# Performance work log

Measured on AMD Instinct MI355X. Metric: run time of the kernel, lower is better.

The kernel has to match this reference:

```python
import jax, jax.numpy as jnp
import numpy as np

H = 8                 # num_heads
SCALE = 25.0          # self.scale
SIM_THRESH = 0.75
CONF_SIM_THRESH = 0.99


def _l2n(x):
    return x / jnp.linalg.norm(x, axis=-1, keepdims=True)


def setup_inputs() -> dict:
    key = jax.random.key(0)
    ks = jax.random.split(key, 10)
    B, N1, N2, C = 1, 512, 2048, 1024
    s = 0.02
    return {
        'x_cls': jax.random.normal(ks[0], (B, N2, C), jnp.float32),
        'x_reg': jax.random.normal(ks[1], (B, N2, C), jnp.float32),
        'cls_score': jax.random.uniform(ks[2], (N2,), dtype=jnp.float32),
        'fg_score': jax.random.uniform(ks[3], (N2,), dtype=jnp.float32),
        'W_q_cls': jax.random.normal(ks[4], (C, C), jnp.float32) * s,
        'W_kv_cls': jax.random.normal(ks[5], (C, 2 * C), jnp.float32) * s,
        'W_q_reg': jax.random.normal(ks[6], (C, C), jnp.float32) * s,
        'W_kv_reg': jax.random.normal(ks[7], (C, 2 * C), jnp.float32) * s,
        'W_lin': jax.random.normal(ks[8], (2 * C, 2 * C), jnp.float32) * s,
        'b_lin': jnp.zeros((2 * C,), jnp.float32),
        'W_lin_reg': jax.random.normal(ks[9], (2 * C, 2 * C), jnp.float32) * s,
        'b_lin_reg': jnp.zeros((2 * C,), jnp.float32),
        'local_preds_num': 512,
    }


def _forward(x_cls, x_reg, cls_score, fg_score, W_q_cls, W_kv_cls, W_q_reg, W_kv_reg,
             W_lin, b_lin, W_lin_reg, b_lin_reg, N1):
    B, N2, C = x_cls.shape
    hd = C // H
    # QKV projections (torch Linear with bias=False; weights stored [in,out])
    q_cls = (x_cls[:, :N1] @ W_q_cls).reshape(B, N1, H, hd).transpose(0, 2, 1, 3)   # [B,H,N1,hd]
    kv = (x_cls @ W_kv_cls).reshape(B, N2, 2, H, hd).transpose(2, 0, 3, 1, 4)
    k_cls, v_cls = kv[0], kv[1]                                                      # [B,H,N2,hd]
    q_reg = (x_reg[:, :N1] @ W_q_reg).reshape(B, N1, H, hd).transpose(0, 2, 1, 3)
    kv = (x_reg @ W_kv_reg).reshape(B, N2, 2, H, hd).transpose(2, 0, 3, 1, 4)
    k_reg, v_reg = kv[0], kv[1]
    # L2 normalization of q, k and of v for raw similarity
    q_cls, k_cls = _l2n(q_cls), _l2n(k_cls)
    q_reg, k_reg = _l2n(q_reg), _l2n(k_reg)
    v_cls_n, v_reg_n = _l2n(v_cls), _l2n(v_reg)
    # per-key score broadcast over [1,H,N1,N2] (use_mask=False path)
    cs = cls_score.reshape(1, 1, 1, N2)
    # raw value-value similarity
    attn_cls_raw = jnp.einsum('bhqd,bhkd->bhqk', v_cls_n[:, :, :N1], v_cls_n)        # [B,H,N1,N2]
    attn_reg_raw = jnp.einsum('bhqd,bhkd->bhqk', v_reg_n[:, :, :N1], v_reg_n)
    # blended softmax attention (attn_drop=0 -> identity)
    attn_cls = jax.nn.softmax(jnp.einsum('bhqd,bhkd->bhqk', q_cls, k_cls) * SCALE * cs, axis=-1)
    attn_reg = jax.nn.softmax(jnp.einsum('bhqd,bhkd->bhqk', q_reg, k_reg) * SCALE, axis=-1)
    attn = (attn_cls + attn_reg) * 0.5
    # attended features + original local values, then output linears
    x = jnp.einsum('bhqk,bhkd->bhqd', attn, v_cls).transpose(0, 2, 1, 3).reshape(B, N1, C)
    x_ori = v_cls[:, :, :N1].transpose(0, 2, 1, 3).reshape(B, N1, C)
    out_cls = jnp.concatenate([x, x_ori], axis=-1) @ W_lin + b_lin                   # [B,N1,2C]
    xr = jnp.einsum('bhqk,bhkd->bhqd', attn, v_reg).transpose(0, 2, 1, 3).reshape(B, N1, C)
    xr_ori = v_reg[:, :, :N1].transpose(0, 2, 1, 3).reshape(B, N1, C)
    out_reg = jnp.concatenate([xr, xr_ori], axis=-1) @ W_lin_reg + b_lin_reg         # reconf=True
    # ave branch: similarity-masked renormalized second-round averaging (batch 0)
    sim_mask = (attn_cls_raw.sum(axis=1)[0] / H > SIM_THRESH).astype(x_cls.dtype)    # [N1,N2]
    obj_mask = (attn_reg_raw.sum(axis=1)[0] / H > CONF_SIM_THRESH).astype(x_cls.dtype)
    sim_round2 = jax.nn.softmax(attn.sum(axis=1)[0] / H, axis=-1)
    sim_round2 = sim_mask * sim_round2
    sim_round2 = sim_round2 / sim_round2.sum(axis=-1, keepdims=True)
    obj_w = obj_mask * sim_round2
    obj_w = obj_w / obj_w.sum(axis=-1, keepdims=True)
    support_cls = v_cls.transpose(0, 2, 1, 3).reshape(B, N2, C)[0]                   # [N2,C]
    support_reg = v_reg.transpose(0, 2, 1, 3).reshape(B, N2, C)[0]
    cls_feature = jnp.concatenate([sim_round2 @ support_cls, out_cls[0]], axis=-1)   # [N1,3C]
    reg_feature = jnp.concatenate([obj_w @ support_reg, out_reg[0]], axis=-1)        # [N1,3C]
    return cls_feature, reg_feature


def reference(x_cls, x_reg, cls_score, fg_score, W_q_cls, W_kv_cls, W_q_reg, W_kv_reg,
              W_lin, b_lin, W_lin_reg, b_lin_reg, local_preds_num):
    return _forward(x_cls, x_reg, cls_score, fg_score, W_q_cls, W_kv_cls, W_q_reg,
                    W_kv_reg, W_lin, b_lin, W_lin_reg, b_lin_reg, local_preds_num)
```

## Files before the change

kernel.cpp:

```cpp
#include <hip/hip_runtime.h>

typedef _Float16 half8 __attribute__((ext_vector_type(8)));
typedef _Float16 half4v __attribute__((ext_vector_type(4)));
typedef float f32x4 __attribute__((ext_vector_type(4)));

#define GLD16(gptr, lptr) \
    __builtin_amdgcn_global_load_lds((const __attribute__((address_space(1))) void*)(gptr), \
                                     (__attribute__((address_space(3))) void*)(lptr), 16, 0, 0)

#define WAIT_VM3   0x0F73
#define WAIT_VM0   0x0F70
#define WAIT_LGKM0 0xC07F

struct GD {
    const _Float16* A; const _Float16* B; void* C;
    const float* colScale;
    _Float16 *vnp, *vtp, *xop;
    long sAh, sAg, sBh, sBg, sSplit, sCh, sCg;
    int lda, ldb, ldc, K, SK, hmask, hshift;
    int ahx, outHalf, csMode, nx, ny, normMode;
    float alpha;
};

__global__ __launch_bounds__(512, 4)
void hgemm3(GD d0, GD d1, int zSplit)
{
    const bool second = (int)blockIdx.z >= zSplit;
    const GD& d = second ? d1 : d0;
    const int bz = second ? (int)blockIdx.z - zSplit : (int)blockIdx.z;
    if ((int)blockIdx.x >= d.nx || (int)blockIdx.y >= d.ny) return;

    __shared__ uint4 smem[4608];
    char* sb = (char*)smem;
    const int tid = threadIdx.x;
    const int w = tid >> 6, l = tid & 63;
    const int m0 = blockIdx.y << 8, n0 = blockIdx.x << 7;
    const int wm = (w >> 1) << 6, wn = (w & 1) << 6;
    const int kq = l >> 4, lm = l & 15;

    const int zz = bz / d.SK, s = bz - zz * d.SK;
    const int h = d.ahx ? (int)blockIdx.x : (zz & d.hmask);
    const int g = d.ahx ? zz : (zz >> d.hshift);
    const _Float16* A = d.A + (long)h * d.sAh + (long)g * d.sAg;
    const _Float16* B = d.B + (long)h * d.sBh + (long)g * d.sBg;
    const long Coff = (long)s * d.sSplit + (long)h * d.sCh + (long)g * d.sCg;
    const int kper = d.K / d.SK, kbeg = s * kper;
    const int NT = kper >> 5;

    const int rS = (w << 4) + (l >> 2);
    const int cS = (l & 3) ^ ((l >> 3) & 3);
    const _Float16* gA0 = A + (long)(m0 + rS) * d.lda + kbeg + cS * 8;
    const _Float16* gB0 = B + (long)(n0 + rS) * d.ldb + kbeg + cS * 8;
    const int lo = w * 1024 + l * 16;

    auto stage = [&](int t) {
        char* dst = sb + (t % 3) * 24576;
        GLD16(gA0 + t * 32,                     dst + lo);
        GLD16(gA0 + (long)128 * d.lda + t * 32, dst + 8192 + lo);
        GLD16(gB0 + t * 32,                     dst + 16384 + lo);
    };

    f32x4 acc[4][4] = {};
    stage(0);
    if (NT > 1) stage(1);
    if (NT > 1) __builtin_amdgcn_s_waitcnt(WAIT_VM3);
    else        __builtin_amdgcn_s_waitcnt(WAIT_VM0);
    __builtin_amdgcn_s_barrier();

    const int sw16 = ((kq ^ ((lm >> 1) & 3)) << 4);
    for (int t = 0; t < NT; ++t) {
        const char* cb = sb + (t % 3) * 24576;
        half8 af[4], bfr[4];
        const char* pa = cb + (wm + lm) * 64 + sw16;
        const char* pb = cb + 16384 + (wn + lm) * 64 + sw16;
        #pragma unroll
        for (int i = 0; i < 4; ++i) {
            af[i]  = *(const half8*)(pa + i * 1024);
            bfr[i] = *(const half8*)(pb + i * 1024);
        }
        #pragma unroll
        for (int mi = 0; mi < 4; ++mi)
            #pragma unroll
            for (int ni = 0; ni < 4; ++ni)
                acc[mi][ni] = __builtin_amdgcn_mfma_f32_16x16x32_f16(af[mi], bfr[ni], acc[mi][ni], 0, 0, 0);
        __builtin_amdgcn_s_waitcnt(WAIT_LGKM0);
        if (t + 2 < NT) { stage(t + 2); __builtin_amdgcn_s_waitcnt(WAIT_VM3); }
        else if (t + 1 < NT) __builtin_amdgcn_s_waitcnt(WAIT_VM0);
        __builtin_amdgcn_s_barrier();
    }

    if (d.normMode == 0) {
        const int rbase = m0 + wm + kq * 4;
        #pragma unroll
        for (int mi = 0; mi < 4; ++mi) {
            #pragma unroll
            for (int ni = 0; ni < 4; ++ni) {
                const int col = n0 + wn + ni * 16 + lm;
                float cs = d.alpha;
                if (d.csMode == 1 || (d.csMode == 2 && g == 0)) cs *= d.colScale[col];
                #pragma unroll
                for (int r = 0; r < 4; ++r) {
                    const long row = rbase + mi * 16 + r;
                    const float v = acc[mi][ni][r] * cs;
                    const long off = Coff + row * d.ldc + col;
                    if (d.outHalf) ((_Float16*)d.C)[off] = (_Float16)v;
                    else           ((float*)d.C)[off] = v;
                }
            }
        }
        return;
    }

    float* part = (float*)sb;
    float ssq[4][4];
    #pragma unroll
    for (int mi = 0; mi < 4; ++mi)
        #pragma unroll
        for (int r = 0; r < 4; ++r) {
            float sq = 0.f;
            #pragma unroll
            for (int ni = 0; ni < 4; ++ni) { const float v = acc[mi][ni][r]; sq += v * v; }
            sq += __shfl_xor(sq, 1, 64);
            sq += __shfl_xor(sq, 2, 64);
            sq += __shfl_xor(sq, 4, 64);
            sq += __shfl_xor(sq, 8, 64);
            ssq[mi][r] = sq;
        }
    if (lm == 0) {
        #pragma unroll
        for (int mi = 0; mi < 4; ++mi)
            #pragma unroll
            for (int r = 0; r < 4; ++r)
                part[(w & 1) * 256 + wm + kq * 4 + mi * 16 + r] = ssq[mi][r];
    }
    __syncthreads();

    #pragma unroll
    for (int mi = 0; mi < 4; ++mi) {
        #pragma unroll
        for (int r = 0; r < 4; ++r) {
            const int rl = wm + kq * 4 + mi * 16 + r;
            const float inv = rsqrtf(part[rl] + part[256 + rl]);
            const long rg = m0 + rl;
            if (d.normMode == 1) {
                #pragma unroll
                for (int ni = 0; ni < 4; ++ni) {
                    const int col = n0 + wn + ni * 16 + lm;
                    ((_Float16*)d.C)[(long)g * 524288 + rg * 1024 + col] =
                        (_Float16)(acc[mi][ni][r] * inv);
                }
            } else if (n0 < 1024) {
                #pragma unroll
                for (int ni = 0; ni < 4; ++ni) {
                    const int col = n0 + wn + ni * 16 + lm;
                    ((_Float16*)d.C)[(long)g * 2097152 + rg * 1024 + col] =
                        (_Float16)(acc[mi][ni][r] * inv);
                }
            } else {
                #pragma unroll
                for (int ni = 0; ni < 4; ++ni) {
                    const int nL = n0 - 1024 + wn + ni * 16 + lm;
                    d.vnp[(long)g * 2097152 + rg * 1024 + nL] =
                        (_Float16)(acc[mi][ni][r] * inv);
                    if (rg < 512)
                        d.xop[(long)g * 524288 + rg * 1024 + nL] = (_Float16)acc[mi][ni][r];
                }
            }
        }
    }
    if (d.normMode == 2 && n0 >= 1024) {
        #pragma unroll
        for (int mi = 0; mi < 4; ++mi)
            #pragma unroll
            for (int ni = 0; ni < 4; ++ni) {
                const int nL = n0 - 1024 + wn + ni * 16 + lm;
                half4v t;
                t.x = (_Float16)acc[mi][ni][0]; t.y = (_Float16)acc[mi][ni][1];
                t.z = (_Float16)acc[mi][ni][2]; t.w = (_Float16)acc[mi][ni][3];
                *(half4v*)(d.vtp + (long)g * 2097152 + (long)nL * 2048
                           + m0 + wm + kq * 4 + mi * 16) = t;
            }
    }
}

static GD mkgd(const _Float16* A, const _Float16* B, void* C, const float* cscale,
               long sAh, long sAg, long sBh, long sBg, long sSplit, long sCh, long sCg,
               int lda, int ldb, int ldc, int K, int SK, int hmask, int hshift,
               int ahx, int outHalf, int csMode, int nx, int ny, float alpha)
{
    GD d; d.A=A; d.B=B; d.C=C; d.colScale=cscale;
    d.vnp=nullptr; d.vtp=nullptr; d.xop=nullptr;
    d.sAh=sAh; d.sAg=sAg; d.sBh=sBh; d.sBg=sBg; d.sSplit=sSplit; d.sCh=sCh; d.sCg=sCg;
    d.lda=lda; d.ldb=ldb; d.ldc=ldc; d.K=K; d.SK=SK; d.hmask=hmask; d.hshift=hshift;
    d.ahx=ahx; d.outHalf=outHalf; d.csMode=csMode; d.nx=nx; d.ny=ny; d.normMode=0;
    d.alpha=alpha;
    return d;
}

__global__ __launch_bounds__(256)
void cast_f2h(const float* __restrict__ s0, const float* __restrict__ s1,
              _Float16* __restrict__ d, int n4)
{
    const int i = blockIdx.x * 256 + threadIdx.x;
    const float* s = blockIdx.y ? s1 : s0;
    const float4 v = ((const float4*)s)[i];
    half4v o;
    o.x = (_Float16)v.x; o.y = (_Float16)v.y; o.z = (_Float16)v.z; o.w = (_Float16)v.w;
    ((half4v*)(d + (size_t)blockIdx.y * n4 * 4))[i] = o;
}

__global__ __launch_bounds__(256)
void prep_transpose(const float* __restrict__ Wq_c, const float* __restrict__ Wq_r,
                    const float* __restrict__ Wkv_c, const float* __restrict__ Wkv_r,
                    const float* __restrict__ Wl_c, const float* __restrict__ Wl_r,
                    _Float16* __restrict__ WqT, _Float16* __restrict__ WkvT,
                    _Float16* __restrict__ WlinT)
{
    __shared__ float t[32][33];
    const int z = blockIdx.z;
    const float* src; _Float16* dst; int ldsrc, lddst, nx, ky;
    switch (z) {
        case 0: src=Wq_c;  dst=WqT;            ldsrc=1024; lddst=1024; nx=32; ky=32; break;
        case 1: src=Wq_r;  dst=WqT+1048576;    ldsrc=1024; lddst=1024; nx=32; ky=32; break;
        case 2: src=Wkv_c; dst=WkvT;           ldsrc=2048; lddst=1024; nx=64; ky=32; break;
        case 3: src=Wkv_r; dst=WkvT+2097152;   ldsrc=2048; lddst=1024; nx=64; ky=32; break;
        case 4: src=Wl_c;  dst=WlinT;          ldsrc=2048; lddst=2048; nx=64; ky=64; break;
        default:src=Wl_r;  dst=WlinT+4194304;  ldsrc=2048; lddst=2048; nx=64; ky=64; break;
    }
    if ((int)blockIdx.x >= nx || (int)blockIdx.y >= ky) return;
    const int n0 = blockIdx.x << 5, k0 = blockIdx.y << 5;
    const int tx = threadIdx.x & 31, ty = threadIdx.x >> 5;
    #pragma unroll
    for (int j = ty; j < 32; j += 8)
        t[j][tx] = src[(size_t)(k0 + j) * ldsrc + n0 + tx];
    __syncthreads();
    #pragma unroll
    for (int j = ty; j < 32; j += 8)
        dst[(size_t)(n0 + j) * lddst + k0 + tx] = (_Float16)t[tx][j];
}

template<int OP>
__device__ __forceinline__ float bred(float v, float* lds)
{
    #pragma unroll
    for (int o = 32; o > 0; o >>= 1) {
        const float u = __shfl_xor(v, o, 64);
        v = OP ? fmaxf(v, u) : v + u;
    }
    __syncthreads();
    if ((threadIdx.x & 63) == 0) lds[threadIdx.x >> 6] = v;
    __syncthreads();
    return OP ? fmaxf(fmaxf(lds[0], lds[1]), fmaxf(lds[2], lds[3]))
              : lds[0] + lds[1] + lds[2] + lds[3];
}

__global__ __launch_bounds__(256)
void sb2_kernel(const _Float16* __restrict__ S16, const float* __restrict__ simPart,
                _Float16* __restrict__ attn,
                _Float16* __restrict__ wc, _Float16* __restrict__ wr)
{
    __shared__ float lds[4];
    const int q = blockIdx.x, t = threadIdx.x;
    float asum[8] = {};
    for (int hh = 0; hh < 8; ++hh) {
        const size_t rb = (size_t)(hh * 512 + q) * 2048;
        float vc[8], vr[8];
        float mc = -1e30f, mr = -1e30f;
        #pragma unroll
        for (int j = 0; j < 8; ++j) {
            vc[j] = (float)S16[rb + t + 256 * j];
            vr[j] = (float)S16[8388608 + rb + t + 256 * j];
            mc = fmaxf(mc, vc[j]); mr = fmaxf(mr, vr[j]);
        }
        mc = bred<1>(mc, lds);
        mr = bred<1>(mr, lds);
        float sc = 0.f, sr = 0.f;
        #pragma unroll
        for (int j = 0; j < 8; ++j) {
            vc[j] = expf(vc[j] - mc); sc += vc[j];
            vr[j] = expf(vr[j] - mr); sr += vr[j];
        }
        sc = bred<0>(sc, lds);
        sr = bred<0>(sr, lds);
        const float ic = 0.5f / sc, ir = 0.5f / sr;
        #pragma unroll
        for (int j = 0; j < 8; ++j) {
            const float a = vc[j] * ic + vr[j] * ir;
            attn[rb + t + 256 * j] = (_Float16)a;
            asum[j] += a;
        }
    }
    float mx = -1e30f;
    #pragma unroll
    for (int j = 0; j < 8; ++j) { asum[j] *= 0.125f; mx = fmaxf(mx, asum[j]); }
    mx = bred<1>(mx, lds);
    float em[8], emo[8];
    float s1 = 0.f, s2 = 0.f;
    const size_t qb = (size_t)q * 2048;
    #pragma unroll
    for (int j = 0; j < 8; ++j) {
        const size_t o = qb + t + 256 * j;
        const float sim = simPart[o];
        const float reg = simPart[1048576 + o];
        const float e = expf(asum[j] - mx);
        const float m  = sim > 0.75f ? 1.f : 0.f;
        const float mo = reg > 0.99f ? 1.f : 0.f;
        em[j] = e * m; emo[j] = e * m * mo;
        s1 += em[j]; s2 += emo[j];
    }
    s1 = bred<0>(s1, lds);
    s2 = bred<0>(s2, lds);
    const float i1 = 1.f / s1, i2 = 1.f / s2;
    #pragma unroll
    for (int j = 0; j < 8; ++j) {
        wc[qb + t + 256 * j] = (_Float16)(em[j] * i1);
        wr[qb + t + 256 * j] = (_Float16)(emo[j] * i2);
    }
}

__global__ __launch_bounds__(256)
void build_xcat(const float* __restrict__ xcatPart, const _Float16* __restrict__ x_ori,
                _Float16* __restrict__ xcat)
{
    const int idx = blockIdx.x * 256 + threadIdx.x;
    const int j = idx & 2047;
    const int n = (idx >> 11) & 511;
    const int g = idx >> 20;
    _Float16 v;
    if (j < 1024) {
        float a = 0.f;
        #pragma unroll
        for (int s = 0; s < 4; ++s)
            a += xcatPart[(size_t)s * 1048576 + (size_t)g * 524288 + n * 1024 + j];
        v = (_Float16)a;
    } else {
        v = x_ori[(size_t)g * 524288 + (size_t)n * 1024 + (j - 1024)];
    }
    xcat[idx] = v;
}

__global__ __launch_bounds__(256)
void finalize(const float* __restrict__ avePart, const float* __restrict__ outPart,
              const float* __restrict__ b_lin, const float* __restrict__ b_lin_reg,
              float* __restrict__ out)
{
    const int idx = blockIdx.x * 256 + threadIdx.x;
    const int c = idx % 3072;
    const int r = (idx / 3072) & 511;
    const int g = idx / (3072 * 512);
    float v;
    if (c < 1024) {
        v = 0.f;
        #pragma unroll
        for (int s = 0; s < 4; ++s)
            v += avePart[(size_t)s * 1048576 + (size_t)g * 524288 + r * 1024 + c];
    } else {
        const int cc = c - 1024;
        v = (g ? b_lin_reg : b_lin)[cc];
        #pragma unroll
        for (int s = 0; s < 4; ++s)
            v += outPart[(size_t)s * 2097152 + (size_t)g * 1048576 + r * 2048 + cc];
    }
    out[idx] = v;
}

extern "C" void kernel_launch(void* const* d_in, const int* in_sizes, int n_in,
                              void* d_out, int out_size, void* d_ws, size_t ws_size,
                              hipStream_t stream)
{
    const float* x_cls     = (const float*)d_in[0];
    const float* x_reg     = (const float*)d_in[1];
    const float* cls_score = (const float*)d_in[2];
    const float* W_q_cls   = (const float*)d_in[4];
    const float* W_kv_cls  = (const float*)d_in[5];
    const float* W_q_reg   = (const float*)d_in[6];
    const float* W_kv_reg  = (const float*)d_in[7];
    const float* W_lin     = (const float*)d_in[8];
    const float* b_lin     = (const float*)d_in[9];
    const float* W_lin_reg = (const float*)d_in[10];
    const float* b_lin_reg = (const float*)d_in[11];
    float* out = (float*)d_out;

    if (ws_size < (size_t)124 * 1048576) return;

    char* W = (char*)d_ws;
    auto at = [&](size_t mb) { return (void*)(W + mb * 1048576); };
    _Float16* WlinT   = (_Float16*)at(0);
    _Float16* vT      = (_Float16*)at(16);
    _Float16* x_ori   = (_Float16*)at(24);
    _Float16* w_c     = (_Float16*)at(26);
    _Float16* w_r     = (_Float16*)at(28);
    _Float16* qn      = (_Float16*)at(30);
    float*    simPart = (float*)at(32);
    float*    outPart = (float*)at(32);
    _Float16* kn      = (_Float16*)at(40);
    _Float16* vn      = (_Float16*)at(48);
    _Float16* attn_h  = (_Float16*)at(40);
    _Float16* xbf     = (_Float16*)at(56);
    _Float16* WqT     = (_Float16*)at(64);
    _Float16* xcat16  = (_Float16*)at(64);
    _Float16* WkvT    = (_Float16*)at(68);
    _Float16* S16     = (_Float16*)at(76);
    float*    xcatPart= (float*)at(76);
    float*    avePart = (float*)at(92);

    cast_f2h<<<dim3(2048, 2), 256, 0, stream>>>(x_cls, x_reg, xbf, 524288);
    prep_transpose<<<dim3(64, 64, 6), 256, 0, stream>>>(
        W_q_cls, W_q_reg, W_kv_cls, W_kv_reg, W_lin, W_lin_reg, WqT, WkvT, WlinT);

    {
        GD q  = mkgd(xbf, WqT, qn, nullptr,
                     0, 2097152, 0, 1048576, 0, 0, 0,
                     1024, 1024, 1024, 1024, 1, 0, 0, 1, 0, 0, 8, 2, 1.f);
        q.normMode = 1;
        GD kv = mkgd(xbf, WkvT, kn, nullptr,
                     0, 2097152, 0, 2097152, 0, 0, 0,
                     1024, 1024, 1024, 1024, 1, 0, 0, 1, 0, 0, 16, 8, 1.f);
        kv.normMode = 2; kv.vnp = vn; kv.vtp = vT; kv.xop = x_ori;
        hgemm3<<<dim3(16, 8, 4), 512, 0, stream>>>(q, kv, 2);
    }

    {
        GD vs = mkgd(vn, vn, simPart, nullptr,
                     0, 2097152, 0, 2097152, 0, 0, 1048576,
                     1024, 1024, 2048, 1024, 1, 0, 0, 0, 0, 0, 16, 2, 0.125f);
        GD sc = mkgd(qn, kn, S16, cls_score,
                     128, 524288, 128, 2097152, 0, 1048576, 8388608,
                     1024, 1024, 2048, 128, 1, 7, 3, 0, 1, 2, 16, 2, 25.f);
        hgemm3<<<dim3(16, 2, 18), 512, 0, stream>>>(vs, sc, 2);
    }

    sb2_kernel<<<512, 256, 0, stream>>>(S16, simPart, attn_h, w_c, w_r);

    {
        GD av = mkgd(attn_h, vT, xcatPart, nullptr,
                     1048576, 0, 0, 2097152, 1048576, 0, 524288,
                     2048, 2048, 1024, 2048, 4, 0, 0, 1, 0, 0, 8, 2, 1.f);
        GD ae = mkgd(w_c, vT, avePart, nullptr,
                     0, 1048576, 0, 2097152, 1048576, 0, 524288,
                     2048, 2048, 1024, 2048, 4, 0, 0, 0, 0, 0, 8, 2, 1.f);
        hgemm3<<<dim3(8, 2, 16), 512, 0, stream>>>(av, ae, 8);
    }

    build_xcat<<<8192, 256, 0, stream>>>(xcatPart, x_ori, xcat16);

    {
        GD ol = mkgd(xcat16, WlinT, outPart, nullptr,
                     0, 1048576, 0, 4194304, 2097152, 0, 1048576,
                     2048, 2048, 2048, 2048, 4, 0, 0, 0, 0, 0, 16, 2, 1.f);
        hgemm3<<<dim3(16, 2, 8), 512, 0, stream>>>(ol, ol, 8);
    }

    finalize<<<12288, 256, 0, stream>>>(avePart, outPart, b_lin, b_lin_reg, out);
}
```

Measured before the change: 296.0 us.

## Interleave GEMM LDS reads with MFMA, remap workgroups, merge prep kernels, half partials

The GEMM main loop now splits the B fragment loads into two halves and issues the next global->LDS stage earlier, with sched barriers and s_setprio around the MFMA bursts, so LDS reads overlap with matrix math. Workgroup indices are remapped in groups of eight, which appears intended to spread neighbouring tiles across XCDs/caches. The cast and weight-transpose prep kernels are merged into one launch, and the attention-V split-K partials are stored in fp16 instead of fp32 to cut memory traffic. The fp16 partial sums risk some precision loss, and the remap changes cache locality patterns.

```diff
diff --git a/kernel.cpp b/kernel.cpp
--- a/kernel.cpp
+++ b/kernel.cpp
@@ -28,18 +28,30 @@
     const bool second = (int)blockIdx.z >= zSplit;
     const GD& d = second ? d1 : d0;
     const int bz = second ? (int)blockIdx.z - zSplit : (int)blockIdx.z;
-    if ((int)blockIdx.x >= d.nx || (int)blockIdx.y >= d.ny) return;
+
+    const int GX = gridDim.x, GY = gridDim.y;
+    int bx = (int)blockIdx.x, by = (int)blockIdx.y;
+    {
+        const int NWG = GX * GY;
+        if (d.nx * d.ny == NWG) {
+            const int lin = by * GX + bx;
+            const int q8 = NWG >> 3;
+            const int wg = (lin & 7) * q8 + (lin >> 3);
+            bx = wg % GX; by = wg / GX;
+        }
+    }
+    if (bx >= d.nx || by >= d.ny) return;
 
     __shared__ uint4 smem[4608];
     char* sb = (char*)smem;
     const int tid = threadIdx.x;
     const int w = tid >> 6, l = tid & 63;
-    const int m0 = blockIdx.y << 8, n0 = blockIdx.x << 7;
+    const int m0 = by << 8, n0 = bx << 7;
     const int wm = (w >> 1) << 6, wn = (w & 1) << 6;
     const int kq = l >> 4, lm = l & 15;
 
     const int zz = bz / d.SK, s = bz - zz * d.SK;
-    const int h = d.ahx ? (int)blockIdx.x : (zz & d.hmask);
+    const int h = d.ahx ? bx : (zz & d.hmask);
     const int g = d.ahx ? zz : (zz >> d.hshift);
     const _Float16* A = d.A + (long)h * d.sAh + (long)g * d.sAg;
     const _Float16* B = d.B + (long)h * d.sBh + (long)g * d.sBg;
@@ -70,22 +82,36 @@
     const int sw16 = ((kq ^ ((lm >> 1) & 3)) << 4);
     for (int t = 0; t < NT; ++t) {
         const char* cb = sb + (t % 3) * 24576;
-        half8 af[4], bfr[4];
         const char* pa = cb + (wm + lm) * 64 + sw16;
         const char* pb = cb + 16384 + (wn + lm) * 64 + sw16;
-        #pragma unroll
-        for (int i = 0; i < 4; ++i) {
-            af[i]  = *(const half8*)(pa + i * 1024);
-            bfr[i] = *(const half8*)(pb + i * 1024);
-        }
-        #pragma unroll
-        for (int mi = 0; mi < 4; ++mi)
-            #pragma unroll
-            for (int ni = 0; ni < 4; ++ni)
-                acc[mi][ni] = __builtin_amdgcn_mfma_f32_16x16x32_f16(af[mi], bfr[ni], acc[mi][ni], 0, 0, 0);
+        half8 af[4], bfr[4];
+        bfr[0] = *(const half8*)(pb + 0 * 1024);
+        bfr[1] = *(const half8*)(pb + 1 * 1024);
+        #pragma unroll
+        for (int i = 0; i < 4; ++i) af[i] = *(const half8*)(pa + i * 1024);
+        if (t + 2 < NT) stage(t + 2);
         __builtin_amdgcn_s_waitcnt(WAIT_LGKM0);
-        if (t + 2 < NT) { stage(t + 2); __builtin_amdgcn_s_waitcnt(WAIT_VM3); }
+        __builtin_amdgcn_sched_barrier(0);
+        __builtin_amdgcn_s_setprio(1);
+        #pragma unroll
+        for (int mi = 0; mi < 4; ++mi) {
+            acc[mi][0] = __builtin_amdgcn_mfma_f32_16x16x32_f16(af[mi], bfr[0], acc[mi][0], 0, 0, 0);
+            acc[mi][1] = __builtin_amdgcn_mfma_f32_16x16x32_f16(af[mi], bfr[1], acc[mi][1], 0, 0, 0);
+        }
+        __builtin_amdgcn_s_setprio(0);
+        bfr[2] = *(const half8*)(pb + 2 * 1024);
+        bfr[3] = *(const half8*)(pb + 3 * 1024);
+        if (t + 2 < NT)      __builtin_amdgcn_s_waitcnt(WAIT_VM3);
         else if (t + 1 < NT) __builtin_amdgcn_s_waitcnt(WAIT_VM0);
+        __builtin_amdgcn_s_waitcnt(WAIT_LGKM0);
+        __builtin_amdgcn_sched_barrier(0);
+        __builtin_amdgcn_s_setprio(1);
+        #pragma unroll
+        for (int mi = 0; mi < 4; ++mi) {
+            acc[mi][2] = __builtin_amdgcn_mfma_f32_16x16x32_f16(af[mi], bfr[2], acc[mi][2], 0, 0, 0);
+            acc[mi][3] = __builtin_amdgcn_mfma_f32_16x16x32_f16(af[mi], bfr[3], acc[mi][3], 0, 0, 0);
+        }
+        __builtin_amdgcn_s_setprio(0);
         __builtin_amdgcn_s_barrier();
     }
 
@@ -198,26 +224,27 @@
 }
 
 __global__ __launch_bounds__(256)
-void cast_f2h(const float* __restrict__ s0, const float* __restrict__ s1,
-              _Float16* __restrict__ d, int n4)
-{
-    const int i = blockIdx.x * 256 + threadIdx.x;
-    const float* s = blockIdx.y ? s1 : s0;
-    const float4 v = ((const float4*)s)[i];
-    half4v o;
-    o.x = (_Float16)v.x; o.y = (_Float16)v.y; o.z = (_Float16)v.z; o.w = (_Float16)v.w;
-    ((half4v*)(d + (size_t)blockIdx.y * n4 * 4))[i] = o;
-}
-
-__global__ __launch_bounds__(256)
-void prep_transpose(const float* __restrict__ Wq_c, const float* __restrict__ Wq_r,
-                    const float* __restrict__ Wkv_c, const float* __restrict__ Wkv_r,
-                    const float* __restrict__ Wl_c, const float* __restrict__ Wl_r,
-                    _Float16* __restrict__ WqT, _Float16* __restrict__ WkvT,
-                    _Float16* __restrict__ WlinT)
-{
+void prep_all(const float* __restrict__ x_cls, const float* __restrict__ x_reg,
+              const float* __restrict__ Wq_c, const float* __restrict__ Wq_r,
+              const float* __restrict__ Wkv_c, const float* __restrict__ Wkv_r,
+              const float* __restrict__ Wl_c, const float* __restrict__ Wl_r,
+              _Float16* __restrict__ xbf,
+              _Float16* __restrict__ WqT, _Float16* __restrict__ WkvT,
+              _Float16* __restrict__ WlinT)
+{
+    const int z = blockIdx.z;
+    if (z == 6) {
+        const int lin = blockIdx.y * 64 + blockIdx.x;
+        const int which = lin >> 11;
+        const int i = (lin & 2047) * 256 + threadIdx.x;
+        const float* s = which ? x_reg : x_cls;
+        const float4 v = ((const float4*)s)[i];
+        half4v o;
+        o.x = (_Float16)v.x; o.y = (_Float16)v.y; o.z = (_Float16)v.z; o.w = (_Float16)v.w;
+        ((half4v*)(xbf + (size_t)which * 2097152))[i] = o;
+        return;
+    }
     __shared__ float t[32][33];
-    const int z = blockIdx.z;
     const float* src; _Float16* dst; int ldsrc, lddst, nx, ky;
     switch (z) {
         case 0: src=Wq_c;  dst=WqT;            ldsrc=1024; lddst=1024; nx=32; ky=32; break;
@@ -319,7 +346,7 @@
 }
 
 __global__ __launch_bounds__(256)
-void build_xcat(const float* __restrict__ xcatPart, const _Float16* __restrict__ x_ori,
+void build_xcat(const _Float16* __restrict__ xcatPart, const _Float16* __restrict__ x_ori,
                 _Float16* __restrict__ xcat)
 {
     const int idx = blockIdx.x * 256 + threadIdx.x;
@@ -331,7 +358,7 @@
         float a = 0.f;
         #pragma unroll
         for (int s = 0; s < 4; ++s)
-            a += xcatPart[(size_t)s * 1048576 + (size_t)g * 524288 + n * 1024 + j];
+            a += (float)xcatPart[(size_t)s * 1048576 + (size_t)g * 524288 + n * 1024 + j];
         v = (_Float16)a;
     } else {
         v = x_ori[(size_t)g * 524288 + (size_t)n * 1024 + (j - 1024)];
@@ -401,12 +428,12 @@
     _Float16* xcat16  = (_Float16*)at(64);
     _Float16* WkvT    = (_Float16*)at(68);
     _Float16* S16     = (_Float16*)at(76);
-    float*    xcatPart= (float*)at(76);
-    float*    avePart = (float*)at(92);
-
-    cast_f2h<<<dim3(2048, 2), 256, 0, stream>>>(x_cls, x_reg, xbf, 524288);
-    prep_transpose<<<dim3(64, 64, 6), 256, 0, stream>>>(
-        W_q_cls, W_q_reg, W_kv_cls, W_kv_reg, W_lin, W_lin_reg, WqT, WkvT, WlinT);
+    _Float16* xcatPart= (_Float16*)at(76);
+    float*    avePart = (float*)at(84);
+
+    prep_all<<<dim3(64, 64, 7), 256, 0, stream>>>(
+        x_cls, x_reg, W_q_cls, W_q_reg, W_kv_cls, W_kv_reg, W_lin, W_lin_reg,
+        xbf, WqT, WkvT, WlinT);
 
     {
         GD q  = mkgd(xbf, WqT, qn, nullptr,
@@ -435,7 +462,7 @@
     {
         GD av = mkgd(attn_h, vT, xcatPart, nullptr,
                      1048576, 0, 0, 2097152, 1048576, 0, 524288,
-                     2048, 2048, 1024, 2048, 4, 0, 0, 1, 0, 0, 8, 2, 1.f);
+                     2048, 2048, 1024, 2048, 4, 0, 0, 1, 1, 0, 8, 2, 1.f);
         GD ae = mkgd(w_c, vT, avePart, nullptr,
                      0, 1048576, 0, 2097152, 1048576, 0, 524288,
                      2048, 2048, 1024, 2048, 4, 0, 0, 0, 0, 0, 8, 2, 1.f);
```

Result: faster. 280.7 us (-5.2%).
